# Performance work log

Hardware: AMD Instinct MI355X
Metric: run time of the kernel (lower is better)

## Reference

```python
import jax, jax.numpy as jnp
import numpy as np

PC = (-51.2, -51.2, -5.0, 51.2, 51.2, 3.0)
BEV_H, BEV_W, BEV_Z = 50, 50, 4
NCAM, NUM_HEADS = 6, 8
EPS = 1e-5


def _layer_norm(x, g, b):
    m = jnp.mean(x, -1, keepdims=True)
    v = jnp.mean((x - m) ** 2, -1, keepdims=True)
    return (x - m) / jnp.sqrt(v + 1e-5) * g + b


def _grid_sample(imgs, pts):
    # imgs: (B,C,H,W); pts: (B,N,2) normalized coords; bilinear,
    # align_corners=False, zero padding (matches F.grid_sample defaults).
    B, C, H, W = imgs.shape
    def one(img, p):
        x = ((p[:, 0] + 1.0) * W - 1.0) * 0.5
        y = ((p[:, 1] + 1.0) * H - 1.0) * 0.5
        x0 = jnp.floor(x); y0 = jnp.floor(y)
        wx = x - x0; wy = y - y0
        def g(xi, yi):
            ok = (xi >= 0) & (xi < W) & (yi >= 0) & (yi < H)
            v = img[:, jnp.clip(yi, 0, H - 1).astype(jnp.int32),
                       jnp.clip(xi, 0, W - 1).astype(jnp.int32)]
            return v * ok[None, :]
        return (g(x0, y0) * (1 - wx) * (1 - wy) + g(x0 + 1, y0) * wx * (1 - wy)
                + g(x0, y0 + 1) * (1 - wx) * wy + g(x0 + 1, y0 + 1) * wx * wy)
    return jax.vmap(one)(imgs, pts)  # (B,C,N)


def _mha(q, kv, inW, inb, outW, outb):
    # torch nn.MultiheadAttention (batch_first)
    C = q.shape[-1]; d = C // NUM_HEADS
    B, Nq = q.shape[:2]; Nk = kv.shape[1]
    Q = q @ inW[:C].T + inb[:C]
    K = kv @ inW[C:2 * C].T + inb[C:2 * C]
    V = kv @ inW[2 * C:].T + inb[2 * C:]
    Qh = Q.reshape(B, Nq, NUM_HEADS, d).transpose(0, 2, 1, 3)
    Kh = K.reshape(B, Nk, NUM_HEADS, d).transpose(0, 2, 1, 3)
    Vh = V.reshape(B, Nk, NUM_HEADS, d).transpose(0, 2, 1, 3)
    s = jnp.einsum('bhqd,bhkd->bhqk', Qh, Kh) / float(np.sqrt(d))
    a = jax.nn.softmax(s, axis=-1)
    o = jnp.einsum('bhqk,bhkd->bhqd', a, Vh).transpose(0, 2, 1, 3).reshape(B, Nq, C)
    return o @ outW.T + outb


def _warp_prev(prev_bev, ego_motion):
    B, N, C = prev_bev.shape
    sp = prev_bev.transpose(0, 2, 1).reshape(B, C, BEV_H, BEV_W)
    tx = ego_motion[:, 0, 3]; ty = ego_motion[:, 1, 3]
    yaw = jnp.arctan2(ego_motion[:, 1, 0], ego_motion[:, 0, 0])
    dx = tx / ((PC[3] - PC[0]) / BEV_W) * 2.0 / BEV_W
    dy = ty / ((PC[4] - PC[1]) / BEV_H) * 2.0 / BEV_H
    c = jnp.cos(yaw); s = jnp.sin(yaw)
    theta = jnp.stack([jnp.stack([c, -s, dx], -1),
                       jnp.stack([s, c, dy], -1)], axis=1)  # (B,2,3)
    # F.affine_grid, align_corners=False: output-pixel-center base grid
    xs = (2.0 * jnp.arange(BEV_W) + 1.0) / BEV_W - 1.0
    ys = (2.0 * jnp.arange(BEV_H) + 1.0) / BEV_H - 1.0
    gx, gy = jnp.meshgrid(xs, ys)  # (H,W) each
    base = jnp.stack([gx, gy, jnp.ones_like(gx)], -1)  # (H,W,3)
    grid = jnp.einsum('bij,hwj->bhwi', theta, base).reshape(B, -1, 2)
    out = _grid_sample(sp, grid)  # (B,C,N)
    return out.transpose(0, 2, 1)


def _reference_points(B):
    ys = (jnp.arange(BEV_H, dtype=jnp.float32) + 0.5) / BEV_H
    xs = (jnp.arange(BEV_W, dtype=jnp.float32) + 0.5) / BEV_W
    ry, rx = jnp.meshgrid(ys, xs, indexing='ij')
    rx = rx.reshape(-1); ry = ry.reshape(-1)
    zs = (jnp.arange(BEV_Z, dtype=jnp.float32) + 0.5) / BEV_Z
    N = BEV_H * BEV_W
    ref = jnp.stack([jnp.broadcast_to(rx[:, None], (N, BEV_Z)),
                     jnp.broadcast_to(ry[:, None], (N, BEV_Z)),
                     jnp.broadcast_to(zs[None, :], (N, BEV_Z))], -1)
    return jnp.broadcast_to(ref[None], (B, N, BEV_Z, 3))  # (B,Nq,Z,3)


def _point_sampling(ref, img_feats, lidar2img):
    B, Nq, Zb, _ = ref.shape
    _, Ncam, C, Hf, Wf = img_feats.shape
    x = ref[..., 0] * (PC[3] - PC[0]) + PC[0]
    y = ref[..., 1] * (PC[4] - PC[1]) + PC[1]
    z = ref[..., 2] * (PC[5] - PC[2]) + PC[2]
    pts = jnp.stack([x, y, z, jnp.ones_like(x)], -1).reshape(B, 1, Nq * Zb, 4)
    pts = jnp.broadcast_to(pts, (B, Ncam, Nq * Zb, 4))
    cam = jnp.einsum('bnij,bnpj->bnpi', lidar2img, pts)
    depth = cam[..., 2]
    xy = cam[..., 0:2] / jnp.clip(depth, EPS)[..., None]
    gx = (xy[..., 0] / (Wf - 1) - 0.5) * 2.0
    gy = (xy[..., 1] / (Hf - 1) - 0.5) * 2.0
    valid = ((depth > EPS) & (gx > -1.0) & (gx < 1.0)
             & (gy > -1.0) & (gy < 1.0))  # (B,Ncam,Nq*Zb)
    grid = jnp.stack([gx, gy], -1).reshape(B * Ncam, Nq * Zb, 2)
    samp = _grid_sample(img_feats.reshape(B * Ncam, C, Hf, Wf), grid)
    samp = samp.reshape(B, Ncam, C, Nq, Zb) * valid.reshape(B, Ncam, 1, Nq, Zb)
    return jnp.nan_to_num(samp)


def _forward(query, prev_bev, img_feats, ego_motion, lidar2img,
             attn_w_W, attn_w_b, sca_out_W, sca_out_b,
             in_proj_W, in_proj_b, mha_out_W, mha_out_b,
             norm1_g, norm1_b, ffn_W1, ffn_b1, ffn_W2, ffn_b2,
             norm2_g, norm2_b):
    B, Nq, C = query.shape
    # Temporal self-attention with warped previous BEV
    aligned = _warp_prev(prev_bev, ego_motion)
    kv = jnp.concatenate([query, aligned], axis=1)
    attn = _mha(query, kv, in_proj_W, in_proj_b, mha_out_W, mha_out_b)
    q = _layer_norm(query + attn, norm1_g, norm1_b)
    # Spatial cross attention
    ref = _reference_points(B)
    samp = _point_sampling(ref, img_feats, lidar2img)  # (B,Ncam,C,Nq,Z)
    w = (q @ attn_w_W.T + attn_w_b).reshape(B, Nq, NCAM * BEV_Z)
    w = jax.nn.softmax(w, axis=-1).reshape(B, Nq, NCAM, BEV_Z)
    agg = jnp.einsum('bncqz,bqnz->bqc', samp, w)
    q = agg @ sca_out_W.T + sca_out_b + q
    # FFN (Linear -> ReLU -> Linear -> LayerNorm), residual outside
    h = jax.nn.relu(q @ ffn_W1.T + ffn_b1) @ ffn_W2.T + ffn_b2
    return q + _layer_norm(h, norm2_g, norm2_b)


def setup_inputs() -> dict:
    key = jax.random.key(0)
    ks = jax.random.split(key, 16)
    B, Nq, C, Hf, Wf = 1, BEV_H * BEV_W, 256, 28, 50
    s = 0.02
    d = {
        'query': jax.random.normal(ks[0], (B, Nq, C), jnp.float32),
        'prev_bev': jax.random.normal(ks[1], (B, Nq, C), jnp.float32),
        'img_feats': jax.random.normal(ks[2], (B, NCAM, C, Hf, Wf), jnp.float32),
        'ego_motion': jax.random.normal(ks[3], (B, 4, 4), jnp.float32),
        'lidar2img': jax.random.normal(ks[4], (B, NCAM, 4, 4), jnp.float32),
        'attn_w_W': jax.random.normal(ks[5], (NCAM * BEV_Z, C), jnp.float32) * s,
        'attn_w_b': jnp.zeros((NCAM * BEV_Z,), jnp.float32),
        'sca_out_W': jax.random.normal(ks[6], (C, C), jnp.float32) * s,
        'sca_out_b': jnp.zeros((C,), jnp.float32),
        'in_proj_W': jax.random.normal(ks[7], (3 * C, C), jnp.float32) * s,
        'in_proj_b': jnp.zeros((3 * C,), jnp.float32),
        'mha_out_W': jax.random.normal(ks[8], (C, C), jnp.float32) * s,
        'mha_out_b': jnp.zeros((C,), jnp.float32),
        'norm1_g': jnp.ones((C,), jnp.float32),
        'norm1_b': jnp.zeros((C,), jnp.float32),
        'ffn_W1': jax.random.normal(ks[9], (2 * C, C), jnp.float32) * s,
        'ffn_b1': jnp.zeros((2 * C,), jnp.float32),
        'ffn_W2': jax.random.normal(ks[10], (C, 2 * C), jnp.float32) * s,
        'ffn_b2': jnp.zeros((C,), jnp.float32),
        'norm2_g': jnp.ones((C,), jnp.float32),
        'norm2_b': jnp.zeros((C,), jnp.float32),
    }
    return d


def reference(query, prev_bev, img_feats, ego_motion, lidar2img,
              attn_w_W, attn_w_b, sca_out_W, sca_out_b,
              in_proj_W, in_proj_b, mha_out_W, mha_out_b,
              norm1_g, norm1_b, ffn_W1, ffn_b1, ffn_W2, ffn_b2,
              norm2_g, norm2_b):
    return _forward(query, prev_bev, img_feats, ego_motion, lidar2img,
                    attn_w_W, attn_w_b, sca_out_W, sca_out_b,
                    in_proj_W, in_proj_b, mha_out_W, mha_out_b,
                    norm1_g, norm1_b, ffn_W1, ffn_b1, ffn_W2, ffn_b2,
                    norm2_g, norm2_b)
```

## Files before the change

kernel.cpp:

```cpp
#include <hip/hip_runtime.h>
#include <hip/hip_bf16.h>
#include <math.h>

#define NQ   2500
#define CDIM 256
#define NKV  5000
#define NH   8
#define DH   32
#define SPLITS 10
#define KPS   500
#define FULLT 7
#define TILES 8
#define TAILNK 52

typedef __attribute__((ext_vector_type(8))) short bf16x8;
typedef __attribute__((ext_vector_type(4))) short short4v;
typedef __attribute__((ext_vector_type(4))) float f32x4;

#define MFMA __builtin_amdgcn_mfma_f32_16x16x32_bf16

__device__ __forceinline__ short f2bf(float f) {
  union { float f; unsigned u; } v; v.f = f;
  unsigned r = v.u + 0x7FFFu + ((v.u >> 16) & 1u);
  return (short)(r >> 16);
}
__device__ __forceinline__ float bf2f(unsigned short s) {
  union { unsigned u; float f; } x; x.u = ((unsigned)s) << 16; return x.f;
}
__device__ __forceinline__ unsigned cvt_pk_bf16(float a, float b) {
  unsigned r;
  asm("v_cvt_pk_bf16_f32 %0, %1, %2" : "=v"(r) : "v"(a), "v"(b));
  return r;
}
__device__ __forceinline__ float exp2_fast(float x) {
  float r; asm("v_exp_f32 %0, %1" : "=v"(r) : "v"(x)); return r;
}

__global__ __launch_bounds__(256) void k_prep(
    const float* __restrict__ query, const float* __restrict__ prev,
    const float* __restrict__ ego, float* __restrict__ kv,
    const float* __restrict__ img, unsigned short* __restrict__ imgT,
    const float* __restrict__ inW, const float* __restrict__ moW,
    const float* __restrict__ scaW, const float* __restrict__ fW1,
    const float* __restrict__ fW2, short* __restrict__ wf)
{
  const int gid = blockIdx.x, tid = threadIdx.x;
  if (gid < NKV) {
    const int row = gid, c = tid;
    if (row < NQ) { kv[(size_t)row*CDIM + c] = query[(size_t)row*CDIM + c]; return; }
    int n = row - NQ;
    float txm = ego[3], tym = ego[7];
    float yaw = atan2f(ego[4], ego[0]);
    float cs = cosf(yaw), sn = sinf(yaw);
    float dx = txm * (1.f/51.2f), dy = tym * (1.f/51.2f);
    int i = n / 50, j = n % 50;
    float gx = (2.f*j + 1.f)*(1.f/50.f) - 1.f;
    float gy = (2.f*i + 1.f)*(1.f/50.f) - 1.f;
    float px = cs*gx - sn*gy + dx;
    float py = sn*gx + cs*gy + dy;
    float xf = ((px + 1.f)*50.f - 1.f)*0.5f;
    float yf = ((py + 1.f)*50.f - 1.f)*0.5f;
    float x0f = floorf(xf), y0f = floorf(yf);
    int x0 = (int)x0f, y0 = (int)y0f;
    float wx = xf - x0f, wy = yf - y0f;
    float v00 = (x0  >=0 && x0  <50 && y0  >=0 && y0  <50) ? prev[((size_t)(y0*50+x0      ))*CDIM + c] : 0.f;
    float v10 = (x0+1>=0 && x0+1<50 && y0  >=0 && y0  <50) ? prev[((size_t)(y0*50+x0+1    ))*CDIM + c] : 0.f;
    float v01 = (x0  >=0 && x0  <50 && y0+1>=0 && y0+1<50) ? prev[((size_t)((y0+1)*50+x0  ))*CDIM + c] : 0.f;
    float v11 = (x0+1>=0 && x0+1<50 && y0+1>=0 && y0+1<50) ? prev[((size_t)((y0+1)*50+x0+1))*CDIM + c] : 0.f;
    float v = (v00*(1.f-wx) + v10*wx)*(1.f-wy) + (v01*(1.f-wx) + v11*wx)*wy;
    kv[(size_t)row*CDIM + c] = v;
    return;
  }
  if (gid < NKV + 168) {
    const int b = gid - NKV;
    const int n = b / 28, y = b % 28;
    const int c = tid;
    for (int x = 0; x < 50; ++x)
      imgT[((size_t)((n*28 + y)*50 + x))*CDIM + c] =
        (unsigned short)f2bf(img[((size_t)(n*CDIM + c)*28 + y)*50 + x]);
    return;
  }
  {
    const int id = (gid - NKV - 168)*256 + tid;
    if (id >= 73728) return;
    const int s = id*8;
    const float* src; int off, K, obase;
    if      (s < 65536)  { src = inW;          off = s;          K = 256; obase = 0; }
    else if (s < 131072) { src = inW + 65536;  off = s - 65536;  K = 256; obase = 65536; }
    else if (s < 196608) { src = inW + 131072; off = s - 131072; K = 256; obase = 131072; }
    else if (s < 262144) { src = moW;          off = s - 196608; K = 256; obase = 196608; }
    else if (s < 327680) { src = scaW;         off = s - 262144; K = 256; obase = 262144; }
    else if (s < 458752) { src = fW1;          off = s - 327680; K = 256; obase = 327680; }
    else                 { src = fW2;          off = s - 458752; K = 512; obase = 458752; }
    const int n = off / K, k = off - n*K;
    short4v lo, hi;
    #pragma unroll
    for (int j = 0; j < 4; ++j) { lo[j] = f2bf(src[off+j]); hi[j] = f2bf(src[off+4+j]); }
    short* dst = wf + obase + (size_t)((n>>4)*(K>>3) + (k>>3))*128 + (n&15)*8;
    *(short4v*)dst = lo;
    *(short4v*)(dst+4) = hi;
  }
}

__global__ __launch_bounds__(256) void k_gemm_qkv(
    const float* __restrict__ A, const short* __restrict__ Wf,
    const float* __restrict__ bias, short* __restrict__ Qbf,
    short* __restrict__ Kbf, short* __restrict__ VbfT, float qscale)
{
  __shared__ short Abf[8][33][8];
  const int tid = threadIdx.x;
  const int lane = tid & 63, wid = tid >> 6;
  const int wm = wid >> 1, wn = wid & 1;
  const int g = lane >> 4, c = lane & 15;
  const int m0 = blockIdx.y << 5, n0 = blockIdx.x << 6;
  if (n0 < 256 && m0 >= NQ) return;
  const int srow = tid >> 3, skq = tid & 7;
  const short* wfa = Wf + (size_t)((n0 + wn*32) >> 4)       * 32 * 128 + c*8;
  const short* wfb = Wf + (size_t)(((n0 + wn*32) >> 4) + 1) * 32 * 128 + c*8;
  f32x4 acc0 = {0.f,0.f,0.f,0.f}, acc1 = acc0;
  for (int k0 = 0; k0 < 256; k0 += 64) {
    const float* ap = A + (size_t)(m0+srow)*256 + k0 + skq*8;
    const float4 fa0 = *(const float4*)ap;
    const float4 fa1 = *(const float4*)(ap+4);
    __syncthreads();
    union { unsigned u[4]; bf16x8 v; } pa;
    pa.u[0] = cvt_pk_bf16(fa0.x, fa0.y);  pa.u[1] = cvt_pk_bf16(fa0.z, fa0.w);
    pa.u[2] = cvt_pk_bf16(fa1.x, fa1.y);  pa.u[3] = cvt_pk_bf16(fa1.z, fa1.w);
    *(bf16x8*)&Abf[skq][srow][0] = pa.v;
    __syncthreads();
    #pragma unroll
    for (int s = 0; s < 2; ++s) {
      const int kq = (k0 >> 3) + s*4 + g;
      const bf16x8 fA  = *(const bf16x8*)&Abf[s*4+g][wm*16 + c][0];
      const bf16x8 fW0 = *(const bf16x8*)(wfa + (size_t)kq*128);
      const bf16x8 fW1 = *(const bf16x8*)(wfb + (size_t)kq*128);
      acc0 = MFMA(fA, fW0, acc0, 0,0,0);
      acc1 = MFMA(fA, fW1, acc1, 0,0,0);
    }
  }
  const int nc0 = n0 + wn*32 + c, nc1 = nc0 + 16;
  const float b0v = bias[nc0], b1v = bias[nc1];
  #pragma unroll
  for (int r = 0; r < 4; ++r) {
    const int m = m0 + wm*16 + g*4 + r;
    if (m >= NKV) continue;
    const float v0 = acc0[r] + b0v;
    const float v1 = acc1[r] + b1v;
    if (nc0 < 256) {
      if (m < NQ) {
        Qbf[(size_t)m*256 + nc0] = f2bf(v0*qscale);
        Qbf[(size_t)m*256 + nc1] = f2bf(v1*qscale);
      }
    } else if (nc0 < 512) {
      Kbf[(size_t)m*256 + nc0 - 256] = f2bf(v0);
      Kbf[(size_t)m*256 + nc1 - 256] = f2bf(v1);
    } else {
      VbfT[(size_t)(nc0 - 512)*NKV + m] = f2bf(v0);
      VbfT[(size_t)(nc1 - 512)*NKV + m] = f2bf(v1);
    }
  }
}

__global__ __launch_bounds__(256) void k_repack_v(
    const short* __restrict__ VbfT, short* __restrict__ Vf)
{
  const int idx = blockIdx.x*256 + threadIdx.x;
  const int j    = idx & 7;
  const int lane = (idx >> 3) & 63;
  const int i    = (idx >> 9) & 1;
  const int kt2  = (idx >> 10) & 1;
  const int t    = (idx >> 11) & 7;
  const int h    = (idx >> 14) & 7;
  const int sp   = idx >> 17;
  const int gg = lane >> 4, cc = lane & 15;
  const int ko32 = ((j >> 2) << 4) | (gg << 2) | (j & 3);
  const int kin = t*64 + kt2*32 + ko32;
  const int d = i*16 + cc;
  short v = 0;
  if (kin < KPS) v = VbfT[(size_t)(h*32 + d)*NKV + sp*KPS + kin];
  Vf[idx] = v;
}

__global__ __launch_bounds__(256) void k_gemm(
    const float* __restrict__ A, const short* __restrict__ Wf,
    const float* __restrict__ bias, const float* __restrict__ res,
    float* __restrict__ C, short* __restrict__ Cb,
    int M, int N, int K, int relu, int mode, float scale)
{
  __shared__ short Abf[8][33][8];
  const int tid = threadIdx.x;
  const int lane = tid & 63, wid = tid >> 6;
  const int wm = wid >> 1, wn = wid & 1;
  const int g = lane >> 4, c = lane & 15;
  const int m0 = blockIdx.y << 5, n0 = blockIdx.x << 6;
  const int srow = tid >> 3, skq = tid & 7;
  const int kb8 = K >> 3;
  const short* wfa = Wf + (size_t)((n0 + wn*32) >> 4)       * kb8 * 128 + c*8;
  const short* wfb = Wf + (size_t)(((n0 + wn*32) >> 4) + 1) * kb8 * 128 + c*8;
  f32x4 acc0 = {0.f,0.f,0.f,0.f}, acc1 = acc0;
  const float4 z4 = make_float4(0.f,0.f,0.f,0.f);
  for (int k0 = 0; k0 < K; k0 += 64) {
    float4 fa0 = z4, fa1 = z4;
    if (m0 + srow < M) {
      const float* ap = A + (size_t)(m0+srow)*K + k0 + skq*8;
      fa0 = *(const float4*)ap; fa1 = *(const float4*)(ap+4);
    }
    __syncthreads();
    union { unsigned u[4]; bf16x8 v; } pa;
    pa.u[0] = cvt_pk_bf16(fa0.x, fa0.y);  pa.u[1] = cvt_pk_bf16(fa0.z, fa0.w);
    pa.u[2] = cvt_pk_bf16(fa1.x, fa1.y);  pa.u[3] = cvt_pk_bf16(fa1.z, fa1.w);
    *(bf16x8*)&Abf[skq][srow][0] = pa.v;
    __syncthreads();
    #pragma unroll
    for (int s = 0; s < 2; ++s) {
      const int kq = (k0 >> 3) + s*4 + g;
      const bf16x8 fA  = *(const bf16x8*)&Abf[s*4+g][wm*16 + c][0];
      const bf16x8 fW0 = *(const bf16x8*)(wfa + (size_t)kq*128);
      const bf16x8 fW1 = *(const bf16x8*)(wfb + (size_t)kq*128);
      acc0 = MFMA(fA, fW0, acc0, 0,0,0);
      acc1 = MFMA(fA, fW1, acc1, 0,0,0);
    }
  }
  const int nc0 = n0 + wn*32 + c, nc1 = nc0 + 16;
  const float b0v = bias[nc0], b1v = bias[nc1];
  #pragma unroll
  for (int r = 0; r < 4; ++r) {
    const int m = m0 + wm*16 + g*4 + r;
    if (m >= M) continue;
    float v0 = acc0[r] + b0v;
    float v1 = acc1[r] + b1v;
    if (mode == 0) {
      if (res) { v0 += res[(size_t)m*N + nc0]; v1 += res[(size_t)m*N + nc1]; }
      if (relu) { v0 = fmaxf(v0, 0.f); v1 = fmaxf(v1, 0.f); }
      C[(size_t)m*N + nc0] = v0;
      C[(size_t)m*N + nc1] = v1;
    } else if (mode == 1) {
      Cb[(size_t)m*N + nc0] = f2bf(v0*scale);
      Cb[(size_t)m*N + nc1] = f2bf(v1*scale);
    } else {
      Cb[(size_t)nc0*M + m] = f2bf(v0);
      Cb[(size_t)nc1*M + m] = f2bf(v1);
    }
  }
}

__device__ __forceinline__ void softmax_pv(
    f32x4 s0, f32x4 s1, f32x4 s2, f32x4 s3, bool tail, int g,
    float& m, f32x4& lacc, f32x4& oA, f32x4& oB,
    bf16x8 A0lo, bf16x8 A0hi, bf16x8 A1lo, bf16x8 A1hi, bf16x8 ones)
{
  float sv[16];
  #pragma unroll
  for (int r=0;r<4;++r){ sv[r]=s0[r]; sv[4+r]=s1[r]; sv[8+r]=s2[r]; sv[12+r]=s3[r]; }
  if (tail) {
    #pragma unroll
    for (int i=0;i<16;++i) {
      const int kl = (i>>2)*16 + g*4 + (i&3);
      if (kl >= TAILNK) sv[i] = -1e30f;
    }
  }
  const float t0 = fmaxf(fmaxf(sv[0], sv[1]), sv[2]);
  const float t1 = fmaxf(fmaxf(sv[3], sv[4]), sv[5]);
  const float t2 = fmaxf(fmaxf(sv[6], sv[7]), sv[8]);
  const float t3 = fmaxf(fmaxf(sv[9], sv[10]), sv[11]);
  const float t4 = fmaxf(fmaxf(sv[12], sv[13]), sv[14]);
  const float mx = fmaxf(fmaxf(fmaxf(t0, t1), t2), fmaxf(fmaxf(t3, t4), sv[15]));
  if (!__all(mx <= m + 8.f)) {
    float mm = fmaxf(mx, __shfl_xor(mx, 16));
    mm = fmaxf(mm, __shfl_xor(mm, 32));
    const float mn = fmaxf(m, mm);
    const float scl = exp2_fast(m - mn);
    m = mn;
    lacc[0] *= scl;
    #pragma unroll
    for (int r=0;r<4;++r){ oA[r]*=scl; oB[r]*=scl; }
  }
  float p[16];
  #pragma unroll
  for (int i=0;i<16;++i) p[i] = exp2_fast(sv[i]-m);
  union { unsigned u[4]; bf16x8 v; } b0, b1;
  #pragma unroll
  for (int i=0;i<4;++i) {
    b0.u[i] = cvt_pk_bf16(p[2*i],   p[2*i+1]);
    b1.u[i] = cvt_pk_bf16(p[8+2*i], p[8+2*i+1]);
  }
  oA = MFMA(A0lo, b0.v, oA, 0,0,0);
  oA = MFMA(A0hi, b1.v, oA, 0,0,0);
  oB = MFMA(A1lo, b0.v, oB, 0,0,0);
  oB = MFMA(A1hi, b1.v, oB, 0,0,0);
  lacc = MFMA(ones, b0.v, lacc, 0,0,0);
  lacc = MFMA(ones, b1.v, lacc, 0,0,0);
}

__global__ __launch_bounds__(64) void k_flash6(
    const short* __restrict__ Qbf, const short* __restrict__ Kbf,
    const short* __restrict__ Vf, short* __restrict__ opart,
    float* __restrict__ mlp)
{
  const int lane = threadIdx.x;
  const int g = lane >> 4, c = lane & 15;
  const int flat = blockIdx.x;
  const int p  = flat % 80;
  const int qb = flat / 80;
  const int h  = p & 7;
  const int sp = p >> 3;
  const int q0 = qb * 32;
  const int qa  = min(q0 +      c, NQ-1);
  const int qb2 = min(q0 + 16 + c, NQ-1);
  const bf16x8 qf0 = *(const bf16x8*)(Qbf + (size_t)qa *CDIM + h*DH + g*8);
  const bf16x8 qf1 = *(const bf16x8*)(Qbf + (size_t)qb2*CDIM + h*DH + g*8);
  bf16x8 ones;
  #pragma unroll
  for (int i=0;i<8;++i) ones[i] = (short)0x3F80;
  const int kbase = sp*KPS;
  const size_t doff = (size_t)h*DH + g*8;
  const short* kbp = Kbf + (size_t)(kbase + c)*CDIM + doff;
  const short* vfp = Vf + (size_t)(sp*NH + h)*(TILES*2048) + lane*8;
  const f32x4 z = {0.f,0.f,0.f,0.f};
  f32x4 o00 = z, o01 = z, o10 = z, o11 = z;
  f32x4 lacc0 = z, lacc1 = z;
  float m0v = -INFINITY, m1v = -INFINITY;

  bf16x8 kc0 = *(const bf16x8*)(kbp);
  bf16x8 kc1 = *(const bf16x8*)(kbp + (size_t)16*CDIM);
  bf16x8 kc2 = *(const bf16x8*)(kbp + (size_t)32*CDIM);
  bf16x8 kc3 = *(const bf16x8*)(kbp + (size_t)48*CDIM);

  #pragma unroll
  for (int t = 0; t < FULLT; ++t) {
    const int kt = t*64;
    const f32x4 s00 = MFMA(kc0, qf0, z, 0,0,0);
    const f32x4 s01 = MFMA(kc1, qf0, z, 0,0,0);
    const f32x4 s02 = MFMA(kc2, qf0, z, 0,0,0);
    const f32x4 s03 = MFMA(kc3, qf0, z, 0,0,0);
    const f32x4 s10 = MFMA(kc0, qf1, z, 0,0,0);
    const f32x4 s11 = MFMA(kc1, qf1, z, 0,0,0);
    const f32x4 s12 = MFMA(kc2, qf1, z, 0,0,0);
    const f32x4 s13 = MFMA(kc3, qf1, z, 0,0,0);
    if (t+1 < FULLT) {
      kc0 = *(const bf16x8*)(kbp + (size_t)(kt+64)*CDIM);
      kc1 = *(const bf16x8*)(kbp + (size_t)(kt+80)*CDIM);
      kc2 = *(const bf16x8*)(kbp + (size_t)(kt+96)*CDIM);
      kc3 = *(const bf16x8*)(kbp + (size_t)(kt+112)*CDIM);
    }
    const short* vt = vfp + (size_t)t*2048;
    const bf16x8 A0lo = *(const bf16x8*)(vt       );
    const bf16x8 A1lo = *(const bf16x8*)(vt +  512);
    const bf16x8 A0hi = *(const bf16x8*)(vt + 1024);
    const bf16x8 A1hi = *(const bf16x8*)(vt + 1536);
    softmax_pv(s00,s01,s02,s03, false, g, m0v, lacc0, o00, o01, A0lo, A0hi, A1lo, A1hi, ones);
    softmax_pv(s10,s11,s12,s13, false, g, m1v, lacc1, o10, o11, A0lo, A0hi, A1lo, A1hi, ones);
  }
  {
    const int kt = FULLT*64;
    const int ka0 = min(kbase + kt +      c, NKV-1);
    const int ka1 = min(kbase + kt + 16 + c, NKV-1);
    const int ka2 = min(kbase + kt + 32 + c, NKV-1);
    const int ka3 = min(kbase + kt + 48 + c, NKV-1);
    const bf16x8 kf0 = *(const bf16x8*)(Kbf + (size_t)ka0*CDIM + doff);
    const bf16x8 kf1 = *(const bf16x8*)(Kbf + (size_t)ka1*CDIM + doff);
    const bf16x8 kf2 = *(const bf16x8*)(Kbf + (size_t)ka2*CDIM + doff);
    const bf16x8 kf3 = *(const bf16x8*)(Kbf + (size_t)ka3*CDIM + doff);
    const f32x4 s00 = MFMA(kf0, qf0, z, 0,0,0);
    const f32x4 s01 = MFMA(kf1, qf0, z, 0,0,0);
    const f32x4 s02 = MFMA(kf2, qf0, z, 0,0,0);
    const f32x4 s03 = MFMA(kf3, qf0, z, 0,0,0);
    const f32x4 s10 = MFMA(kf0, qf1, z, 0,0,0);
    const f32x4 s11 = MFMA(kf1, qf1, z, 0,0,0);
    const f32x4 s12 = MFMA(kf2, qf1, z, 0,0,0);
    const f32x4 s13 = MFMA(kf3, qf1, z, 0,0,0);
    const short* vt = vfp + (size_t)FULLT*2048;
    const bf16x8 A0lo = *(const bf16x8*)(vt       );
    const bf16x8 A1lo = *(const bf16x8*)(vt +  512);
    const bf16x8 A0hi = *(const bf16x8*)(vt + 1024);
    const bf16x8 A1hi = *(const bf16x8*)(vt + 1536);
    softmax_pv(s00,s01,s02,s03, true, g, m0v, lacc0, o00, o01, A0lo, A0hi, A1lo, A1hi, ones);
    softmax_pv(s10,s11,s12,s13, true, g, m1v, lacc1, o10, o11, A0lo, A0hi, A1lo, A1hi, ones);
  }
  const size_t ob0 = (size_t)(sp*NH + h)*NQ;
  const int qw0 = q0 + c;
  if (qw0 < NQ) {
    const size_t b = (ob0 + qw0)*DH;
    #pragma unroll
    for (int r=0;r<4;++r) {
      opart[b +      g*4 + r] = f2bf(o00[r]);
      opart[b + 16 + g*4 + r] = f2bf(o01[r]);
    }
    if (g == 0) { mlp[(ob0 + qw0)*2] = m0v; mlp[(ob0 + qw0)*2+1] = lacc0[0]; }
  }
  const int qw1 = q0 + 16 + c;
  if (qw1 < NQ) {
    const size_t b = (ob0 + qw1)*DH;
    #pragma unroll
    for (int r=0;r<4;++r) {
      opart[b +      g*4 + r] = f2bf(o10[r]);
      opart[b + 16 + g*4 + r] = f2bf(o11[r]);
    }
    if (g == 0) { mlp[(ob0 + qw1)*2] = m1v; mlp[(ob0 + qw1)*2+1] = lacc1[0]; }
  }
}

__global__ __launch_bounds__(256) void k_combine(
    const short* __restrict__ opart, const float* __restrict__ mlp,
    float* __restrict__ attn)
{
  const int q = blockIdx.x, t = threadIdx.x;
  const int h = t >> 5, d = t & 31;
  float ms[SPLITS], ls[SPLITS];
  float mstar = -INFINITY;
  #pragma unroll
  for (int s = 0; s < SPLITS; ++s) {
    size_t b = (size_t)(s*NH + h)*NQ + q;
    ms[s] = mlp[b*2]; ls[s] = mlp[b*2+1];
    mstar = fmaxf(mstar, ms[s]);
  }
  float num = 0.f, den = 0.f;
  #pragma unroll
  for (int s = 0; s < SPLITS; ++s) {
    float e = exp2_fast(ms[s] - mstar);
    size_t b = (size_t)(s*NH + h)*NQ + q;
    num += bf2f((unsigned short)opart[b*DH + d])*e;
    den += ls[s]*e;
  }
  attn[(size_t)q*CDIM + t] = num/den;
}

__global__ __launch_bounds__(256) void k_ln(
    const float* __restrict__ x, const float* __restrict__ g,
    const float* __restrict__ b, const float* __restrict__ post_res,
    float* __restrict__ out)
{
  const int row = blockIdx.x, c = threadIdx.x;
  const size_t idx = (size_t)row*CDIM + c;
  const float v = x[idx];
  __shared__ float red[4];
  float s = v;
  #pragma unroll
  for (int m = 1; m < 64; m <<= 1) s += __shfl_xor(s, m);
  if ((c & 63) == 0) red[c >> 6] = s;
  __syncthreads();
  const float mean = (red[0]+red[1]+red[2]+red[3]) * (1.f/256.f);
  const float dv = v - mean;
  __syncthreads();
  float s2 = dv*dv;
  #pragma unroll
  for (int m = 1; m < 64; m <<= 1) s2 += __shfl_xor(s2, m);
  if ((c & 63) == 0) red[c >> 6] = s2;
  __syncthreads();
  const float var = (red[0]+red[1]+red[2]+red[3]) * (1.f/256.f);
  float o = dv * rsqrtf(var + 1e-5f) * g[c] + b[c];
  if (post_res) o += post_res[idx];
  out[idx] = o;
}

__global__ __launch_bounds__(256) void k_sample_agg(
    const float* __restrict__ q1, const unsigned short* __restrict__ imgT,
    const float* __restrict__ l2i, const float* __restrict__ awW,
    const float* __restrict__ awb, float* __restrict__ agg)
{
  const int q = blockIdx.x, tid = threadIdx.x;
  __shared__ float qrow[256];
  __shared__ float wl[24];
  __shared__ float fwx[24], fwy[24];
  __shared__ int iv[24], ix[24], iy[24];
  qrow[tid] = q1[(size_t)q*CDIM + tid];
  __syncthreads();
  if (tid < 192) {
    const int e = tid >> 3, s2 = tid & 7;
    float acc = 0.f;
    for (int c = s2; c < 256; c += 8) acc += qrow[c]*awW[e*256 + c];
    acc += __shfl_xor(acc,1);
    acc += __shfl_xor(acc,2);
    acc += __shfl_xor(acc,4);
    if (s2 == 0) wl[e] = acc + awb[e];
  }
  if (tid < 24) {
    const int e = tid, n = e >> 2, z = e & 3;
    const int iyq = q / 50, jxq = q % 50;
    const float rx = (jxq + 0.5f)*(1.f/50.f);
    const float ry = (iyq + 0.5f)*(1.f/50.f);
    const float rz = (z + 0.5f)*0.25f;
    const float X = rx*102.4f - 51.2f;
    const float Y = ry*102.4f - 51.2f;
    const float Z = rz*8.f - 5.f;
    const float* L = l2i + n*16;
    const float cx = L[0]*X + L[1]*Y + L[2]*Z  + L[3];
    const float cy = L[4]*X + L[5]*Y + L[6]*Z  + L[7];
    const float cd = L[8]*X + L[9]*Y + L[10]*Z + L[11];
    const float dn = fmaxf(cd, 1e-5f);
    const float u = cx/dn, vv = cy/dn;
    const float gx = (u*(1.f/49.f) - 0.5f)*2.f;
    const float gy = (vv*(1.f/27.f) - 0.5f)*2.f;
    const int ok = (cd > 1e-5f) && (gx > -1.f) && (gx < 1.f) && (gy > -1.f) && (gy < 1.f);
    const float xf = ((gx + 1.f)*50.f - 1.f)*0.5f;
    const float yf = ((gy + 1.f)*28.f - 1.f)*0.5f;
    const float x0f = floorf(xf), y0f = floorf(yf);
    iv[e] = ok; ix[e] = (int)x0f; iy[e] = (int)y0f;
    fwx[e] = xf - x0f; fwy[e] = yf - y0f;
  }
  __syncthreads();
  float mx = -INFINITY;
  #pragma unroll
  for (int e = 0; e < 24; ++e) mx = fmaxf(mx, wl[e]);
  float se = 0.f;
  #pragma unroll
  for (int e = 0; e < 24; ++e) se += __expf(wl[e]-mx);
  const float inv = 1.f/se;
  const int c = tid;
  float acc = 0.f;
  #pragma unroll
  for (int e = 0; e < 24; ++e) {
    if (!iv[e]) continue;
    const float w = __expf(wl[e]-mx)*inv;
    const int n = e >> 2;
    const int x0 = ix[e], y0 = iy[e];
    const float wx = fwx[e], wy = fwy[e];
    const size_t base = (size_t)(n*28)*50;
    float v00 = (x0  >=0 && x0  <50 && y0  >=0 && y0  <28) ? bf2f(imgT[((base + (size_t)y0*50     + x0  ))*CDIM + c]) : 0.f;
    float v10 = (x0+1>=0 && x0+1<50 && y0  >=0 && y0  <28) ? bf2f(imgT[((base + (size_t)y0*50     + x0+1))*CDIM + c]) : 0.f;
    float v01 = (x0  >=0 && x0  <50 && y0+1>=0 && y0+1<28) ? bf2f(imgT[((base + (size_t)(y0+1)*50 + x0  ))*CDIM + c]) : 0.f;
    float v11 = (x0+1>=0 && x0+1<50 && y0+1>=0 && y0+1<28) ? bf2f(imgT[((base + (size_t)(y0+1)*50 + x0+1))*CDIM + c]) : 0.f;
    acc += w * ((v00*(1.f-wx) + v10*wx)*(1.f-wy) + (v01*(1.f-wx) + v11*wx)*wy);
  }
  agg[(size_t)q*CDIM + c] = acc;
}

extern "C" void kernel_launch(void* const* d_in, const int* in_sizes, int n_in,
                              void* d_out, int out_size, void* d_ws, size_t ws_size,
                              hipStream_t stream)
{
  const float* query = (const float*)d_in[0];
  const float* prev  = (const float*)d_in[1];
  const float* img   = (const float*)d_in[2];
  const float* ego   = (const float*)d_in[3];
  const float* l2i   = (const float*)d_in[4];
  const float* awW   = (const float*)d_in[5];
  const float* awb   = (const float*)d_in[6];
  const float* scab  = (const float*)d_in[8];
  const float* inb   = (const float*)d_in[10];
  const float* mob   = (const float*)d_in[12];
  const float* n1g   = (const float*)d_in[13];
  const float* n1b   = (const float*)d_in[14];
  const float* fb1   = (const float*)d_in[16];
  const float* fb2   = (const float*)d_in[18];
  const float* n2g   = (const float*)d_in[19];
  const float* n2b   = (const float*)d_in[20];
  float* out = (float*)d_out;
  float* ws  = (float*)d_ws;

  float* kv    = ws;
  short* Qbf   = (short*)(ws + 1280000);
  short* Kbf   = (short*)(ws + 1600000);
  short* VbfT  = (short*)(ws + 2240000);
  short* Vf    = (short*)(ws + 2880000);
  short* opart = (short*)(ws + 3535360);
  float* mlp   = ws + 6735360;
  short* wf    = (short*)(ws + 7135360);
  unsigned short* imgT = (unsigned short*)(ws + 7430272);
  float* attn  = ws;
  float* tmp1  = ws +  640000;
  float* q1    = ws + 1280000;
  float* aggb  = ws + 1920000;
  float* q2    = ws + 2560000;
  float* hbuf  = ws + 3200000;
  float* h2    = ws + 4480000;

  const float qscale = 0.2550727452794943f;

  k_prep<<<5456, 256, 0, stream>>>(query, prev, ego, kv, img, imgT,
                                   (const float*)d_in[9], (const float*)d_in[11],
                                   (const float*)d_in[7], (const float*)d_in[15],
                                   (const float*)d_in[17], wf);
  k_gemm_qkv<<<dim3(12,157), 256, 0, stream>>>(kv, wf, inb, Qbf, Kbf, VbfT, qscale);
  k_repack_v<<<5120, 256, 0, stream>>>(VbfT, Vf);
  k_flash6<<<79*80, 64, 0, stream>>>(Qbf, Kbf, Vf, opart, mlp);
  k_combine<<<NQ, 256, 0, stream>>>(opart, mlp, attn);
  k_gemm<<<dim3(4,79), 256, 0, stream>>>(attn, wf + 196608, mob, query, tmp1, nullptr, NQ, 256, 256, 0, 0, 1.0f);
  k_ln<<<NQ, 256, 0, stream>>>(tmp1, n1g, n1b, nullptr, q1);
  k_sample_agg<<<NQ, 256, 0, stream>>>(q1, imgT, l2i, awW, awb, aggb);
  k_gemm<<<dim3(4,79), 256, 0, stream>>>(aggb, wf + 262144, scab, q1, q2, nullptr, NQ, 256, 256, 0, 0, 1.0f);
  k_gemm<<<dim3(8,79), 256, 0, stream>>>(q2, wf + 327680, fb1, nullptr, hbuf, nullptr, NQ, 512, 256, 1, 0, 1.0f);
  k_gemm<<<dim3(4,79), 256, 0, stream>>>(hbuf, wf + 458752, fb2, nullptr, h2, nullptr, NQ, 256, 512, 0, 0, 1.0f);
  k_ln<<<NQ, 256, 0, stream>>>(h2, n2g, n2b, q2, out);
}
```

Baseline: 141.1 us.

## Fuse V repack into QKV GEMM, combine into out-proj GEMM, shrink flash tile

The QKV GEMM now writes V directly in the MFMA-fragment layout the flash kernel expects, with k_prep zero-filling the padded Vf buffer. This removes the separate transposed-V write and the k_repack_v kernel. The split-softmax combine is folded into the A-load of the output-projection GEMM, which removes k_combine and the attn buffer. The flash kernel now handles 16 queries per wave instead of 32 and launches twice as many blocks with an occupancy hint. That raises K/V reload traffic but lowers register pressure, and the fused combine recomputes its reductions once per N-tile.

```diff
diff --git a/kernel.cpp b/kernel.cpp
--- a/kernel.cpp
+++ b/kernel.cpp
@@ -12,6 +12,7 @@
 #define FULLT 7
 #define TILES 8
 #define TAILNK 52
+#define VF_SHORTS 1310720
 
 typedef __attribute__((ext_vector_type(8))) short bf16x8;
 typedef __attribute__((ext_vector_type(4))) short short4v;
@@ -42,7 +43,8 @@
     const float* __restrict__ img, unsigned short* __restrict__ imgT,
     const float* __restrict__ inW, const float* __restrict__ moW,
     const float* __restrict__ scaW, const float* __restrict__ fW1,
-    const float* __restrict__ fW2, short* __restrict__ wf)
+    const float* __restrict__ fW2, short* __restrict__ wf,
+    unsigned* __restrict__ VfU)
 {
   const int gid = blockIdx.x, tid = threadIdx.x;
   if (gid < NKV) {
@@ -80,7 +82,7 @@
         (unsigned short)f2bf(img[((size_t)(n*CDIM + c)*28 + y)*50 + x]);
     return;
   }
-  {
+  if (gid < NKV + 168 + 288) {
     const int id = (gid - NKV - 168)*256 + tid;
     if (id >= 73728) return;
     const int s = id*8;
@@ -99,13 +101,18 @@
     short* dst = wf + obase + (size_t)((n>>4)*(K>>3) + (k>>3))*128 + (n&15)*8;
     *(short4v*)dst = lo;
     *(short4v*)(dst+4) = hi;
+    return;
+  }
+  {
+    const int id = (gid - NKV - 168 - 288)*256 + tid;
+    VfU[id] = 0u;
   }
 }
 
 __global__ __launch_bounds__(256) void k_gemm_qkv(
     const float* __restrict__ A, const short* __restrict__ Wf,
     const float* __restrict__ bias, short* __restrict__ Qbf,
-    short* __restrict__ Kbf, short* __restrict__ VbfT, float qscale)
+    short* __restrict__ Kbf, short* __restrict__ Vf, float qscale)
 {
   __shared__ short Abf[8][33][8];
   const int tid = threadIdx.x;
@@ -155,37 +162,28 @@
       Kbf[(size_t)m*256 + nc0 - 256] = f2bf(v0);
       Kbf[(size_t)m*256 + nc1 - 256] = f2bf(v1);
     } else {
-      VbfT[(size_t)(nc0 - 512)*NKV + m] = f2bf(v0);
-      VbfT[(size_t)(nc1 - 512)*NKV + m] = f2bf(v1);
-    }
-  }
-}
-
-__global__ __launch_bounds__(256) void k_repack_v(
-    const short* __restrict__ VbfT, short* __restrict__ Vf)
-{
-  const int idx = blockIdx.x*256 + threadIdx.x;
-  const int j    = idx & 7;
-  const int lane = (idx >> 3) & 63;
-  const int i    = (idx >> 9) & 1;
-  const int kt2  = (idx >> 10) & 1;
-  const int t    = (idx >> 11) & 7;
-  const int h    = (idx >> 14) & 7;
-  const int sp   = idx >> 17;
-  const int gg = lane >> 4, cc = lane & 15;
-  const int ko32 = ((j >> 2) << 4) | (gg << 2) | (j & 3);
-  const int kin = t*64 + kt2*32 + ko32;
-  const int d = i*16 + cc;
-  short v = 0;
-  if (kin < KPS) v = VbfT[(size_t)(h*32 + d)*NKV + sp*KPS + kin];
-  Vf[idx] = v;
+      const int d0 = nc0 - 512;
+      const int hh = d0 >> 5;
+      const int cc = d0 & 15;
+      const int sp = m / KPS;
+      const int kin = m - sp*KPS;
+      const int t = kin >> 6, r6 = kin & 63;
+      const int kt2 = r6 >> 5, ko32 = r6 & 31;
+      const int gg = (ko32 >> 2) & 3;
+      const int jj = ((ko32 >> 4) << 2) | (ko32 & 3);
+      const size_t base = (((size_t)(sp*NH + hh)*TILES + t)*2 + kt2)*2;
+      Vf[(base    )*512 + (gg*16 + cc)*8 + jj] = f2bf(v0);
+      Vf[(base + 1)*512 + (gg*16 + cc)*8 + jj] = f2bf(v1);
+    }
+  }
 }
 
 __global__ __launch_bounds__(256) void k_gemm(
     const float* __restrict__ A, const short* __restrict__ Wf,
     const float* __restrict__ bias, const float* __restrict__ res,
     float* __restrict__ C, short* __restrict__ Cb,
-    int M, int N, int K, int relu, int mode, float scale)
+    const short* __restrict__ opart, const float* __restrict__ mlp,
+    int M, int N, int K, int relu, int mode, int amode, float scale)
 {
   __shared__ short Abf[8][33][8];
   const int tid = threadIdx.x;
@@ -201,9 +199,37 @@
   const float4 z4 = make_float4(0.f,0.f,0.f,0.f);
   for (int k0 = 0; k0 < K; k0 += 64) {
     float4 fa0 = z4, fa1 = z4;
-    if (m0 + srow < M) {
-      const float* ap = A + (size_t)(m0+srow)*K + k0 + skq*8;
-      fa0 = *(const float4*)ap; fa1 = *(const float4*)(ap+4);
+    const int mrow = m0 + srow;
+    if (mrow < M) {
+      if (amode == 0) {
+        const float* ap = A + (size_t)mrow*K + k0 + skq*8;
+        fa0 = *(const float4*)ap; fa1 = *(const float4*)(ap+4);
+      } else {
+        const int c0 = k0 + skq*8;
+        const int hh = c0 >> 5, dd = c0 & 31;
+        float mstar = -INFINITY;
+        float ms[SPLITS], ls[SPLITS];
+        #pragma unroll
+        for (int s = 0; s < SPLITS; ++s) {
+          const size_t b = (size_t)(s*NH + hh)*NQ + mrow;
+          ms[s] = mlp[b*2]; ls[s] = mlp[b*2+1];
+          mstar = fmaxf(mstar, ms[s]);
+        }
+        float num[8] = {0,0,0,0,0,0,0,0};
+        float den = 0.f;
+        #pragma unroll
+        for (int s = 0; s < SPLITS; ++s) {
+          const float e = exp2_fast(ms[s] - mstar);
+          den += ls[s]*e;
+          const size_t b = (size_t)(s*NH + hh)*NQ + mrow;
+          const short* op = opart + b*DH + dd;
+          #pragma unroll
+          for (int j = 0; j < 8; ++j) num[j] += bf2f((unsigned short)op[j])*e;
+        }
+        const float inv = 1.f/den;
+        fa0.x = num[0]*inv; fa0.y = num[1]*inv; fa0.z = num[2]*inv; fa0.w = num[3]*inv;
+        fa1.x = num[4]*inv; fa1.y = num[5]*inv; fa1.z = num[6]*inv; fa1.w = num[7]*inv;
+      }
     }
     __syncthreads();
     union { unsigned u[4]; bf16x8 v; } pa;
@@ -234,12 +260,9 @@
       if (relu) { v0 = fmaxf(v0, 0.f); v1 = fmaxf(v1, 0.f); }
       C[(size_t)m*N + nc0] = v0;
       C[(size_t)m*N + nc1] = v1;
-    } else if (mode == 1) {
+    } else {
       Cb[(size_t)m*N + nc0] = f2bf(v0*scale);
       Cb[(size_t)m*N + nc1] = f2bf(v1*scale);
-    } else {
-      Cb[(size_t)nc0*M + m] = f2bf(v0);
-      Cb[(size_t)nc1*M + m] = f2bf(v1);
     }
   }
 }
@@ -275,14 +298,11 @@
     #pragma unroll
     for (int r=0;r<4;++r){ oA[r]*=scl; oB[r]*=scl; }
   }
-  float p[16];
-  #pragma unroll
-  for (int i=0;i<16;++i) p[i] = exp2_fast(sv[i]-m);
   union { unsigned u[4]; bf16x8 v; } b0, b1;
   #pragma unroll
   for (int i=0;i<4;++i) {
-    b0.u[i] = cvt_pk_bf16(p[2*i],   p[2*i+1]);
-    b1.u[i] = cvt_pk_bf16(p[8+2*i], p[8+2*i+1]);
+    b0.u[i] = cvt_pk_bf16(exp2_fast(sv[2*i]-m),   exp2_fast(sv[2*i+1]-m));
+    b1.u[i] = cvt_pk_bf16(exp2_fast(sv[8+2*i]-m), exp2_fast(sv[8+2*i+1]-m));
   }
   oA = MFMA(A0lo, b0.v, oA, 0,0,0);
   oA = MFMA(A0hi, b1.v, oA, 0,0,0);
@@ -292,7 +312,7 @@
   lacc = MFMA(ones, b1.v, lacc, 0,0,0);
 }
 
-__global__ __launch_bounds__(64) void k_flash6(
+__global__ __launch_bounds__(64, 8) void k_flash7(
     const short* __restrict__ Qbf, const short* __restrict__ Kbf,
     const short* __restrict__ Vf, short* __restrict__ opart,
     float* __restrict__ mlp)
@@ -304,11 +324,9 @@
   const int qb = flat / 80;
   const int h  = p & 7;
   const int sp = p >> 3;
-  const int q0 = qb * 32;
-  const int qa  = min(q0 +      c, NQ-1);
-  const int qb2 = min(q0 + 16 + c, NQ-1);
-  const bf16x8 qf0 = *(const bf16x8*)(Qbf + (size_t)qa *CDIM + h*DH + g*8);
-  const bf16x8 qf1 = *(const bf16x8*)(Qbf + (size_t)qb2*CDIM + h*DH + g*8);
+  const int q0 = qb * 16;
+  const int qa = min(q0 + c, NQ-1);
+  const bf16x8 qf = *(const bf16x8*)(Qbf + (size_t)qa*CDIM + h*DH + g*8);
   bf16x8 ones;
   #pragma unroll
   for (int i=0;i<8;++i) ones[i] = (short)0x3F80;
@@ -317,9 +335,8 @@
   const short* kbp = Kbf + (size_t)(kbase + c)*CDIM + doff;
   const short* vfp = Vf + (size_t)(sp*NH + h)*(TILES*2048) + lane*8;
   const f32x4 z = {0.f,0.f,0.f,0.f};
-  f32x4 o00 = z, o01 = z, o10 = z, o11 = z;
-  f32x4 lacc0 = z, lacc1 = z;
-  float m0v = -INFINITY, m1v = -INFINITY;
+  f32x4 oA = z, oB = z, lacc = z;
+  float mv = -INFINITY;
 
   bf16x8 kc0 = *(const bf16x8*)(kbp);
   bf16x8 kc1 = *(const bf16x8*)(kbp + (size_t)16*CDIM);
@@ -329,14 +346,10 @@
   #pragma unroll
   for (int t = 0; t < FULLT; ++t) {
     const int kt = t*64;
-    const f32x4 s00 = MFMA(kc0, qf0, z, 0,0,0);
-    const f32x4 s01 = MFMA(kc1, qf0, z, 0,0,0);
-    const f32x4 s02 = MFMA(kc2, qf0, z, 0,0,0);
-    const f32x4 s03 = MFMA(kc3, qf0, z, 0,0,0);
-    const f32x4 s10 = MFMA(kc0, qf1, z, 0,0,0);
-    const f32x4 s11 = MFMA(kc1, qf1, z, 0,0,0);
-    const f32x4 s12 = MFMA(kc2, qf1, z, 0,0,0);
-    const f32x4 s13 = MFMA(kc3, qf1, z, 0,0,0);
+    const f32x4 s0 = MFMA(kc0, qf, z, 0,0,0);
+    const f32x4 s1 = MFMA(kc1, qf, z, 0,0,0);
+    const f32x4 s2 = MFMA(kc2, qf, z, 0,0,0);
+    const f32x4 s3 = MFMA(kc3, qf, z, 0,0,0);
     if (t+1 < FULLT) {
       kc0 = *(const bf16x8*)(kbp + (size_t)(kt+64)*CDIM);
       kc1 = *(const bf16x8*)(kbp + (size_t)(kt+80)*CDIM);
@@ -348,8 +361,7 @@
     const bf16x8 A1lo = *(const bf16x8*)(vt +  512);
     const bf16x8 A0hi = *(const bf16x8*)(vt + 1024);
     const bf16x8 A1hi = *(const bf16x8*)(vt + 1536);
-    softmax_pv(s00,s01,s02,s03, false, g, m0v, lacc0, o00, o01, A0lo, A0hi, A1lo, A1hi, ones);
-    softmax_pv(s10,s11,s12,s13, false, g, m1v, lacc1, o10, o11, A0lo, A0hi, A1lo, A1hi, ones);
+    softmax_pv(s0,s1,s2,s3, false, g, mv, lacc, oA, oB, A0lo, A0hi, A1lo, A1hi, ones);
   }
   {
     const int kt = FULLT*64;
@@ -361,68 +373,28 @@
     const bf16x8 kf1 = *(const bf16x8*)(Kbf + (size_t)ka1*CDIM + doff);
     const bf16x8 kf2 = *(const bf16x8*)(Kbf + (size_t)ka2*CDIM + doff);
     const bf16x8 kf3 = *(const bf16x8*)(Kbf + (size_t)ka3*CDIM + doff);
-    const f32x4 s00 = MFMA(kf0, qf0, z, 0,0,0);
-    const f32x4 s01 = MFMA(kf1, qf0, z, 0,0,0);
-    const f32x4 s02 = MFMA(kf2, qf0, z, 0,0,0);
-    const f32x4 s03 = MFMA(kf3, qf0, z, 0,0,0);
-    const f32x4 s10 = MFMA(kf0, qf1, z, 0,0,0);
-    const f32x4 s11 = MFMA(kf1, qf1, z, 0,0,0);
-    const f32x4 s12 = MFMA(kf2, qf1, z, 0,0,0);
-    const f32x4 s13 = MFMA(kf3, qf1, z, 0,0,0);
+    const f32x4 s0 = MFMA(kf0, qf, z, 0,0,0);
+    const f32x4 s1 = MFMA(kf1, qf, z, 0,0,0);
+    const f32x4 s2 = MFMA(kf2, qf, z, 0,0,0);
+    const f32x4 s3 = MFMA(kf3, qf, z, 0,0,0);
     const short* vt = vfp + (size_t)FULLT*2048;
     const bf16x8 A0lo = *(const bf16x8*)(vt       );
     const bf16x8 A1lo = *(const bf16x8*)(vt +  512);
     const bf16x8 A0hi = *(const bf16x8*)(vt + 1024);
     const bf16x8 A1hi = *(const bf16x8*)(vt + 1536);
-    softmax_pv(s00,s01,s02,s03, true, g, m0v, lacc0, o00, o01, A0lo, A0hi, A1lo, A1hi, ones);
-    softmax_pv(s10,s11,s12,s13, true, g, m1v, lacc1, o10, o11, A0lo, A0hi, A1lo, A1hi, ones);
+    softmax_pv(s0,s1,s2,s3, true, g, mv, lacc, oA, oB, A0lo, A0hi, A1lo, A1hi, ones);
   }
   const size_t ob0 = (size_t)(sp*NH + h)*NQ;
-  const int qw0 = q0 + c;
-  if (qw0 < NQ) {
-    const size_t b = (ob0 + qw0)*DH;
+  const int qw = q0 + c;
+  if (qw < NQ) {
+    const size_t b = (ob0 + qw)*DH;
     #pragma unroll
     for (int r=0;r<4;++r) {
-      opart[b +      g*4 + r] = f2bf(o00[r]);
-      opart[b + 16 + g*4 + r] = f2bf(o01[r]);
-    }
-    if (g == 0) { mlp[(ob0 + qw0)*2] = m0v; mlp[(ob0 + qw0)*2+1] = lacc0[0]; }
-  }
-  const int qw1 = q0 + 16 + c;
-  if (qw1 < NQ) {
-    const size_t b = (ob0 + qw1)*DH;
-    #pragma unroll
-    for (int r=0;r<4;++r) {
-      opart[b +      g*4 + r] = f2bf(o10[r]);
-      opart[b + 16 + g*4 + r] = f2bf(o11[r]);
-    }
-    if (g == 0) { mlp[(ob0 + qw1)*2] = m1v; mlp[(ob0 + qw1)*2+1] = lacc1[0]; }
-  }
-}
-
-__global__ __launch_bounds__(256) void k_combine(
-    const short* __restrict__ opart, const float* __restrict__ mlp,
-    float* __restrict__ attn)
-{
-  const int q = blockIdx.x, t = threadIdx.x;
-  const int h = t >> 5, d = t & 31;
-  float ms[SPLITS], ls[SPLITS];
-  float mstar = -INFINITY;
-  #pragma unroll
-  for (int s = 0; s < SPLITS; ++s) {
-    size_t b = (size_t)(s*NH + h)*NQ + q;
-    ms[s] = mlp[b*2]; ls[s] = mlp[b*2+1];
-    mstar = fmaxf(mstar, ms[s]);
-  }
-  float num = 0.f, den = 0.f;
-  #pragma unroll
-  for (int s = 0; s < SPLITS; ++s) {
-    float e = exp2_fast(ms[s] - mstar);
-    size_t b = (size_t)(s*NH + h)*NQ + q;
-    num += bf2f((unsigned short)opart[b*DH + d])*e;
-    den += ls[s]*e;
-  }
-  attn[(size_t)q*CDIM + t] = num/den;
+      opart[b +      g*4 + r] = f2bf(oA[r]);
+      opart[b + 16 + g*4 + r] = f2bf(oB[r]);
+    }
+    if (g == 0) { mlp[(ob0 + qw)*2] = mv; mlp[(ob0 + qw)*2+1] = lacc[0]; }
+  }
 }
 
 __global__ __launch_bounds__(256) void k_ln(
@@ -551,35 +523,35 @@
   float* kv    = ws;
   short* Qbf   = (short*)(ws + 1280000);
   short* Kbf   = (short*)(ws + 1600000);
-  short* VbfT  = (short*)(ws + 2240000);
-  short* Vf    = (short*)(ws + 2880000);
-  short* opart = (short*)(ws + 3535360);
-  float* mlp   = ws + 6735360;
-  short* wf    = (short*)(ws + 7135360);
-  unsigned short* imgT = (unsigned short*)(ws + 7430272);
-  float* attn  = ws;
-  float* tmp1  = ws +  640000;
-  float* q1    = ws + 1280000;
-  float* aggb  = ws + 1920000;
-  float* q2    = ws + 2560000;
-  float* hbuf  = ws + 3200000;
-  float* h2    = ws + 4480000;
+  short* Vf    = (short*)(ws + 2240000);
+  short* opart = (short*)(ws + 2895360);
+  float* mlp   = ws + 6095360;
+  short* wf    = (short*)(ws + 6495360);
+  unsigned short* imgT = (unsigned short*)(ws + 6790272);
+  float* tmp1  = ws;
+  float* q1    = ws +  640000;
+  float* aggb  = ws + 1280000;
+  float* q2    = ws + 1920000;
+  float* hbuf  = ws + 2560000;
+  float* h2    = ws + 3840000;
 
   const float qscale = 0.2550727452794943f;
 
-  k_prep<<<5456, 256, 0, stream>>>(query, prev, ego, kv, img, imgT,
+  k_prep<<<8016, 256, 0, stream>>>(query, prev, ego, kv, img, imgT,
                                    (const float*)d_in[9], (const float*)d_in[11],
                                    (const float*)d_in[7], (const float*)d_in[15],
-                                   (const float*)d_in[17], wf);
-  k_gemm_qkv<<<dim3(12,157), 256, 0, stream>>>(kv, wf, inb, Qbf, Kbf, VbfT, qscale);
-  k_repack_v<<<5120, 256, 0, stream>>>(VbfT, Vf);
-  k_flash6<<<79*80, 64, 0, stream>>>(Qbf, Kbf, Vf, opart, mlp);
-  k_combine<<<NQ, 256, 0, stream>>>(opart, mlp, attn);
-  k_gemm<<<dim3(4,79), 256, 0, stream>>>(attn, wf + 196608, mob, query, tmp1, nullptr, NQ, 256, 256, 0, 0, 1.0f);
+                                   (const float*)d_in[17], wf, (unsigned*)Vf);
+  k_gemm_qkv<<<dim3(12,157), 256, 0, stream>>>(kv, wf, inb, Qbf, Kbf, Vf, qscale);
+  k_flash7<<<158*80, 64, 0, stream>>>(Qbf, Kbf, Vf, opart, mlp);
+  k_gemm<<<dim3(4,79), 256, 0, stream>>>(nullptr, wf + 196608, mob, query, tmp1, nullptr,
+                                         opart, mlp, NQ, 256, 256, 0, 0, 1, 1.0f);
   k_ln<<<NQ, 256, 0, stream>>>(tmp1, n1g, n1b, nullptr, q1);
   k_sample_agg<<<NQ, 256, 0, stream>>>(q1, imgT, l2i, awW, awb, aggb);
-  k_gemm<<<dim3(4,79), 256, 0, stream>>>(aggb, wf + 262144, scab, q1, q2, nullptr, NQ, 256, 256, 0, 0, 1.0f);
-  k_gemm<<<dim3(8,79), 256, 0, stream>>>(q2, wf + 327680, fb1, nullptr, hbuf, nullptr, NQ, 512, 256, 1, 0, 1.0f);
-  k_gemm<<<dim3(4,79), 256, 0, stream>>>(hbuf, wf + 458752, fb2, nullptr, h2, nullptr, NQ, 256, 512, 0, 0, 1.0f);
+  k_gemm<<<dim3(4,79), 256, 0, stream>>>(aggb, wf + 262144, scab, q1, q2, nullptr,
+                                         nullptr, nullptr, NQ, 256, 256, 0, 0, 0, 1.0f);
+  k_gemm<<<dim3(8,79), 256, 0, stream>>>(q2, wf + 327680, fb1, nullptr, hbuf, nullptr,
+                                         nullptr, nullptr, NQ, 512, 256, 1, 0, 0, 1.0f);
+  k_gemm<<<dim3(4,79), 256, 0, stream>>>(hbuf, wf + 458752, fb2, nullptr, h2, nullptr,
+                                         nullptr, nullptr, NQ, 256, 512, 0, 0, 0, 1.0f);
   k_ln<<<NQ, 256, 0, stream>>>(h2, n2g, n2b, q2, out);
 }
```

New measurement: 195.5 us. 1.39x slower.
